# Kernel tuning notes

Hardware: AMD Instinct MI355X
Metric: run time of the kernel (lower is better)

Reference implementation:

```python
import jax, jax.numpy as jnp
import numpy as np

N_NODES = 100000
N_EDGES = 1600000
H_IN = 128
H_OUT = 128
ELU_ALPHA = 0.1


def setup_inputs() -> dict:
    key = jax.random.key(0)
    k = jax.random.split(key, 6)
    x = jax.random.normal(k[0], (N_NODES, H_IN), dtype=jnp.float32)
    edge_index = jax.random.randint(k[1], (2, N_EDGES), 0, N_NODES, dtype=jnp.int64)
    s = 1.0 / np.sqrt(H_IN)
    W_conv = jax.random.uniform(k[2], (H_IN, H_OUT), jnp.float32, -s, s)
    b_conv = jnp.zeros((H_OUT,), jnp.float32)
    W_skip = jax.random.uniform(k[3], (H_IN, H_OUT), jnp.float32, -s, s)
    b_skip = jax.random.uniform(k[4], (H_OUT,), jnp.float32, -s, s)
    return {"x": x, "edge_index": edge_index, "W_conv": W_conv,
            "b_conv": b_conv, "W_skip": W_skip, "b_skip": b_skip}


def reference(x, edge_index, W_conv, b_conv, W_skip, b_skip):
    # GCNConv(improved=True): add self-loops with weight 2.0, symmetric norm.
    N = x.shape[0]
    src, dst = edge_index[0], edge_index[1]
    # degree = incoming edge weights (1.0 each) + 2.0 self-loop weight
    deg = jnp.zeros((N,), x.dtype).at[dst].add(1.0) + 2.0
    dinv = jax.lax.rsqrt(deg)                     # deg >= 2 always
    norm = dinv[src] * dinv[dst]                  # [E]
    h = x @ W_conv                                # [N, H_OUT]
    # scatter-add of normalized messages over real edges
    agg = jax.ops.segment_sum(norm[:, None] * h[src], dst, num_segments=N)
    # self-loop contribution: weight 2 * dinv[i]^2
    agg = agg + (2.0 * dinv * dinv)[:, None] * h
    out = agg + b_conv + x @ W_skip + b_skip
    # Dropout(p=0.1) in eval mode = identity; ELU(alpha=0.1)
    return jnp.where(out > 0, out, ELU_ALPHA * (jnp.exp(out) - 1.0))
```

## Files before the change

### kernel.cpp

```cpp
#include <hip/hip_runtime.h>
#include <hip/hip_bf16.h>
#include <hip/hip_fp16.h>

#define H 128
#define BW 128
#define BSH 7
#define NB 256

typedef __attribute__((ext_vector_type(8))) short short8;
typedef __attribute__((ext_vector_type(4))) float f32x4;

__device__ inline unsigned short f2bf(float f) {
    union { float f; unsigned int u; } v; v.f = f;
    unsigned int r = (v.u + 0x7fffu + ((v.u >> 16) & 1u)) >> 16;
    return (unsigned short)r;
}
__device__ inline float bf2f(unsigned short h) {
    union { unsigned int u; float f; } v; v.u = ((unsigned int)h) << 16;
    return v.f;
}

__global__ __launch_bounds__(256) void quant_hist_kernel(const float* __restrict__ x,
                                                         const float* __restrict__ Wc,
                                                         const float* __restrict__ Ws,
                                                         const int* __restrict__ ei,
                                                         uint* __restrict__ xq,
                                                         float* __restrict__ invs,
                                                         short8* __restrict__ wp,
                                                         int* __restrict__ counts,
                                                         int N, int E, int nbu,
                                                         int chunk, int qb) {
    __shared__ int h[1024];
    if (blockIdx.x >= qb) {
        const int b = blockIdx.x - qb;
        for (int i = threadIdx.x; i < nbu; i += 256) h[i] = 0;
        __syncthreads();
        const int lo = b * chunk;
        const int hi = min(E, lo + chunk);
        for (int e = lo + threadIdx.x; e < hi; e += 256)
            atomicAdd(&h[ei[E + e] >> BSH], 1);
        __syncthreads();
        for (int i = threadIdx.x; i < nbu; i += 256) counts[b * nbu + i] = h[i];
        return;
    }
    int node = blockIdx.x * 8 + (threadIdx.x >> 5);
    if (node < N) {
        int l32 = threadIdx.x & 31;
        float4 v = ((const float4*)x)[node * 32 + l32];
        float m = fmaxf(fmaxf(fabsf(v.x), fabsf(v.y)), fmaxf(fabsf(v.z), fabsf(v.w)));
        #pragma unroll
        for (int mk = 1; mk < 32; mk <<= 1) m = fmaxf(m, __shfl_xor(m, mk));
        m = fmaxf(m, 1e-30f);
        float s = 127.0f / m;
        int q0 = min(255, max(0, (int)rintf(v.x * s) + 128));
        int q1 = min(255, max(0, (int)rintf(v.y * s) + 128));
        int q2 = min(255, max(0, (int)rintf(v.z * s) + 128));
        int q3 = min(255, max(0, (int)rintf(v.w * s) + 128));
        xq[node * 32 + l32] = (uint)q0 | ((uint)q1 << 8) | ((uint)q2 << 16) | ((uint)q3 << 24);
        if (l32 == 0) invs[node] = m / 127.0f;
    }
    if (blockIdx.x < 8) {
        int t = blockIdx.x * 256 + threadIdx.x;
        int lane = t & 63;
        int nt = (t >> 6) & 7;
        int ks = t >> 9;
        int kbase = ks * 32 + (lane >> 4) * 8;
        int col = nt * 16 + (lane & 15);
        short8 whc, whs, wls;
        #pragma unroll
        for (int j = 0; j < 8; ++j) {
            float wc = Wc[(kbase + j) * H + col];
            float ws = Ws[(kbase + j) * H + col];
            unsigned short hc = f2bf(wc);
            unsigned short hs = f2bf(ws);
            whc[j] = (short)hc;
            whs[j] = (short)hs;
            wls[j] = (short)f2bf(ws - bf2f(hs));
        }
        int base = (ks * 8 + nt) * 64 + lane;
        wp[base] = whc;
        wp[2048 + base] = whs;
        wp[4096 + base] = wls;
    }
}

__global__ __launch_bounds__(NB) void p2_scan(const int* __restrict__ counts,
                                              int* __restrict__ scanned,
                                              int* __restrict__ btot, int nbu) {
    __shared__ int s[NB];
    const int k = blockIdx.x, t = threadIdx.x;
    int v = counts[t * nbu + k];
    s[t] = v;
    __syncthreads();
    for (int off = 1; off < NB; off <<= 1) {
        int a = (t >= off) ? s[t - off] : 0;
        __syncthreads();
        s[t] += a;
        __syncthreads();
    }
    scanned[t * nbu + k] = s[t] - v;
    if (t == NB - 1) btot[k] = s[t];
}

__global__ __launch_bounds__(256) void p5_scatter(const int* __restrict__ ei,
                                                  const int* __restrict__ btot,
                                                  const int* __restrict__ scanned,
                                                  int* __restrict__ tmp,
                                                  int* __restrict__ cstart,
                                                  int E, int nbu, int chunk) {
    __shared__ int sc[1024];
    __shared__ int part[256];
    __shared__ int lb[1024];
    const int t = threadIdx.x;
    const int b = blockIdx.x;
    const int base = t * 4;
    int v0 = (base + 0 < nbu) ? btot[base + 0] : 0;
    int v1 = (base + 1 < nbu) ? btot[base + 1] : 0;
    int v2 = (base + 2 < nbu) ? btot[base + 2] : 0;
    int v3 = (base + 3 < nbu) ? btot[base + 3] : 0;
    int s1 = v0 + v1, s2 = s1 + v2, s3 = s2 + v3;
    part[t] = s3;
    __syncthreads();
    for (int off = 1; off < 256; off <<= 1) {
        int a = (t >= off) ? part[t - off] : 0;
        __syncthreads();
        part[t] += a;
        __syncthreads();
    }
    int add = (t > 0) ? part[t - 1] : 0;
    sc[base + 0] = add;
    sc[base + 1] = add + v0;
    sc[base + 2] = add + s1;
    sc[base + 3] = add + s2;
    __syncthreads();
    if (b == 0) {
        for (int k = t; k < nbu; k += 256) cstart[k] = sc[k];
        if (t == 0) cstart[nbu] = E;
    }
    for (int k = t; k < nbu; k += 256) lb[k] = sc[k] + scanned[b * nbu + k];
    __syncthreads();
    const int lo = b * chunk;
    const int hi = min(E, lo + chunk);
    for (int e = lo + t; e < hi; e += 256) {
        int s = ei[e], d = ei[E + e];
        int slot = atomicAdd(&lb[d >> BSH], 1);
        tmp[slot] = ((d & (BW - 1)) << 17) | s;
    }
}

__global__ __launch_bounds__(256) void csra_kernel(const int* __restrict__ tmp,
                                                   const int* __restrict__ cstart,
                                                   const float* __restrict__ invs,
                                                   int* __restrict__ rstart,
                                                   float* __restrict__ dinv,
                                                   float* __restrict__ ainv,
                                                   float* __restrict__ selfw,
                                                   int N, int E) {
    __shared__ int ldeg[BW];
    __shared__ int lscan[BW];
    const int b = blockIdx.x;
    const int nstart = b << BSH;
    const int estart = cstart[b];
    const int eend = cstart[b + 1];
    const int t = threadIdx.x;

    if (t < BW) ldeg[t] = 0;
    __syncthreads();
    for (int i = estart + t; i < eend; i += 256)
        atomicAdd(&ldeg[(tmp[i] >> 17) & (BW - 1)], 1);
    __syncthreads();
    if (t < BW) lscan[t] = ldeg[t];
    __syncthreads();
    #pragma unroll
    for (int off = 1; off < BW; off <<= 1) {
        int a = 0;
        if (t < BW && t >= off) a = lscan[t - off];
        __syncthreads();
        if (t < BW) lscan[t] += a;
        __syncthreads();
    }
    if (t < BW) {
        int excl = lscan[t] - ldeg[t];
        int n = nstart + t;
        if (n < N) {
            float iv = invs[n];
            float dv = rsqrtf((float)ldeg[t] + 2.0f);
            rstart[n] = estart + excl;
            dinv[n] = dv;
            ainv[n] = dv * iv;
            selfw[n] = 2.0f * dv * dv * iv;
        }
    }
    if (b == 0 && t == 0) rstart[N] = E;
}

__global__ __launch_bounds__(256) void csrb_kernel(const int* __restrict__ tmp,
                                                   const int* __restrict__ cstart,
                                                   const int* __restrict__ rstart,
                                                   const float* __restrict__ dinv,
                                                   const float* __restrict__ ainv,
                                                   int* __restrict__ entries,
                                                   unsigned short* __restrict__ wgt,
                                                   int N, int E) {
    __shared__ int lcur[BW];
    __shared__ float ldv[BW];
    const int b = blockIdx.x;
    const int nstart = b << BSH;
    const int t = threadIdx.x;
    if (t < BW) {
        int n = nstart + t;
        lcur[t] = (n < N) ? rstart[n] : 0;
        ldv[t] = (n < N) ? dinv[n] : 0.f;
    }
    __syncthreads();
    const int estart = cstart[b];
    const int eend = cstart[b + 1];
    for (int i = estart + t; i < eend; i += 256) {
        int v = tmp[i];
        int ld = (v >> 17) & (BW - 1);
        int src = v & 0x1FFFF;
        float w = ainv[src] * ldv[ld];
        int slot = atomicAdd(&lcur[ld], 1);
        entries[slot] = src;
        wgt[slot] = __half_as_ushort(__float2half(w));
    }
}

__global__ __launch_bounds__(256) void agg_kernel(const int* __restrict__ entries,
                                                  const unsigned short* __restrict__ wgt,
                                                  const int* __restrict__ rstart,
                                                  const float* __restrict__ selfw,
                                                  const uint* __restrict__ xq,
                                                  unsigned short* __restrict__ z, int N) {
    int node = blockIdx.x * 4 + (threadIdx.x >> 6);
    if (node >= N) return;
    const int lane = threadIdx.x & 63;
    const int l16 = lane & 15;
    const int q4 = lane >> 4;
    const uint2* x2 = (const uint2*)xq;

    int start = rstart[node];
    int end = rstart[node + 1];
    float sw = selfw[node];
    uint2 qs = x2[node * 16 + l16];

    float a0 = 0.f, a1 = 0.f, a2 = 0.f, a3 = 0.f;
    float a4 = 0.f, a5 = 0.f, a6 = 0.f, a7 = 0.f;
    float sumw = 0.f;

    for (int c = start; c < end; c += 64) {
        int rem = end - c;
        int src = 0;
        float w = 0.f;
        if (lane < rem) {
            src = entries[c + lane];
            w = __half2float(__ushort_as_half(wgt[c + lane]));
        }
        int cnt = rem < 64 ? rem : 64;
        int iters = (cnt + 3) >> 2;
        #pragma unroll 4
        for (int t = 0; t < iters; ++t) {
            int idx = 4 * t + q4;
            int ss = __shfl(src, idx);
            float wv = __shfl(w, idx);
            uint2 q = x2[ss * 16 + l16];
            sumw += wv;
            a0 += wv * (float)(q.x & 0xffu);
            a1 += wv * (float)((q.x >> 8) & 0xffu);
            a2 += wv * (float)((q.x >> 16) & 0xffu);
            a3 += wv * (float)(q.x >> 24);
            a4 += wv * (float)(q.y & 0xffu);
            a5 += wv * (float)((q.y >> 8) & 0xffu);
            a6 += wv * (float)((q.y >> 16) & 0xffu);
            a7 += wv * (float)(q.y >> 24);
        }
    }

    #define R2(A) A += __shfl_xor(A, 16); A += __shfl_xor(A, 32);
    R2(a0) R2(a1) R2(a2) R2(a3) R2(a4) R2(a5) R2(a6) R2(a7) R2(sumw)
    #undef R2

    if (q4 == 0) {
        sumw += sw;
        a0 += sw * (float)(qs.x & 0xffu);
        a1 += sw * (float)((qs.x >> 8) & 0xffu);
        a2 += sw * (float)((qs.x >> 16) & 0xffu);
        a3 += sw * (float)(qs.x >> 24);
        a4 += sw * (float)(qs.y & 0xffu);
        a5 += sw * (float)((qs.y >> 8) & 0xffu);
        a6 += sw * (float)((qs.y >> 16) & 0xffu);
        a7 += sw * (float)(qs.y >> 24);
        float off = 128.f * sumw;
        uint4 o;
        o.x = (uint)f2bf(a0 - off) | ((uint)f2bf(a1 - off) << 16);
        o.y = (uint)f2bf(a2 - off) | ((uint)f2bf(a3 - off) << 16);
        o.z = (uint)f2bf(a4 - off) | ((uint)f2bf(a5 - off) << 16);
        o.w = (uint)f2bf(a6 - off) | ((uint)f2bf(a7 - off) << 16);
        ((uint4*)z)[node * 16 + l16] = o;
    }
}

__global__ __launch_bounds__(256) void gemm_kernel(const unsigned short* __restrict__ zb,
                                                   const float* __restrict__ x,
                                                   const short8* __restrict__ wp,
                                                   const float* __restrict__ bc,
                                                   const float* __restrict__ bsk,
                                                   float* __restrict__ out, int N) {
    const int lane = threadIdx.x & 63;
    const int wave = threadIdx.x >> 6;
    const int m = lane & 15;
    const int quad = lane >> 4;
    const int row = blockIdx.x * 64 + wave * 16 + m;
    const bool rowok = row < N;

    f32x4 acc[8];
    #pragma unroll
    for (int i = 0; i < 8; ++i) acc[i] = (f32x4){0.f, 0.f, 0.f, 0.f};

    #pragma unroll
    for (int ks = 0; ks < 4; ++ks) {
        const int k0 = ks * 32 + quad * 8;
        short8 za = {0, 0, 0, 0, 0, 0, 0, 0};
        short8 xa_h = {0, 0, 0, 0, 0, 0, 0, 0};
        short8 xa_l = {0, 0, 0, 0, 0, 0, 0, 0};
        if (rowok) {
            za = ((const short8*)zb)[(row * H + k0) >> 3];
            float4 a = *(const float4*)&x[row * H + k0];
            float4 b = *(const float4*)&x[row * H + k0 + 4];
            float xv[8] = {a.x, a.y, a.z, a.w, b.x, b.y, b.z, b.w};
            #pragma unroll
            for (int j = 0; j < 8; ++j) {
                unsigned short h = f2bf(xv[j]);
                xa_h[j] = (short)h;
                xa_l[j] = (short)f2bf(xv[j] - bf2f(h));
            }
        }
        #pragma unroll
        for (int nt = 0; nt < 8; ++nt) {
            int base = (ks * 8 + nt) * 64 + lane;
            short8 bch = wp[base];
            short8 bsh = wp[2048 + base];
            short8 bsl = wp[4096 + base];
            acc[nt] = __builtin_amdgcn_mfma_f32_16x16x32_bf16(za, bch, acc[nt], 0, 0, 0);
            acc[nt] = __builtin_amdgcn_mfma_f32_16x16x32_bf16(xa_h, bsh, acc[nt], 0, 0, 0);
            acc[nt] = __builtin_amdgcn_mfma_f32_16x16x32_bf16(xa_l, bsh, acc[nt], 0, 0, 0);
            acc[nt] = __builtin_amdgcn_mfma_f32_16x16x32_bf16(xa_h, bsl, acc[nt], 0, 0, 0);
        }
    }

    const int orow_base = blockIdx.x * 64 + wave * 16 + quad * 4;
    #pragma unroll
    for (int nt = 0; nt < 8; ++nt) {
        int col = nt * 16 + m;
        float bias = bc[col] + bsk[col];
        #pragma unroll
        for (int r = 0; r < 4; ++r) {
            int orow = orow_base + r;
            if (orow < N) {
                float v = acc[nt][r] + bias;
                v = v > 0.f ? v : 0.1f * (__expf(v) - 1.f);
                out[orow * H + col] = v;
            }
        }
    }
}

extern "C" void kernel_launch(void* const* d_in, const int* in_sizes, int n_in,
                              void* d_out, int out_size, void* d_ws, size_t ws_size,
                              hipStream_t stream) {
    const float* x   = (const float*)d_in[0];
    const int*   ei  = (const int*)d_in[1];
    const float* Wc  = (const float*)d_in[2];
    const float* bc  = (const float*)d_in[3];
    const float* Wsk = (const float*)d_in[4];
    const float* bsk = (const float*)d_in[5];
    float* out = (float*)d_out;

    const int N = in_sizes[0] / H;
    const int E = in_sizes[1] / 2;
    const int nbu = (N + BW - 1) / BW;
    const int chunk = (E + NB - 1) / NB;
    const int qb = (N + 7) / 8;

    char* w = (char*)d_ws;
    short8*         wp      = (short8*)w;
    int*            rstart  = (int*)(w + 131072);
    float*          selfw   = (float*)(w + 589824);
    int*            entries = (int*)(w + 1048576);
    unsigned short* wgt     = (unsigned short*)(w + 7471104);
    uint*           xq      = (uint*)(w + 10747904);
    unsigned short* z       = (unsigned short*)(w + 23592960);
    float*          invs    = (float*)(w + 23592960);
    float*          dinv    = (float*)(w + 23992960);
    float*          ainv    = (float*)(w + 24392960);
    int*            cstart  = (int*)(w + 24792960);
    int*            btot    = (int*)(w + 24796160);
    int*            counts  = (int*)(w + 24799360);
    int*            scanned = (int*)(w + 25600128);
    int*            tmp     = (int*)(w + 26400896);

    quant_hist_kernel<<<qb + NB, 256, 0, stream>>>(x, Wc, Wsk, ei, xq, invs, wp,
                                                   counts, N, E, nbu, chunk, qb);

    p2_scan<<<nbu, NB, 0, stream>>>(counts, scanned, btot, nbu);
    p5_scatter<<<NB, 256, 0, stream>>>(ei, btot, scanned, tmp, cstart, E, nbu, chunk);
    csra_kernel<<<nbu, 256, 0, stream>>>(tmp, cstart, invs, rstart, dinv, ainv, selfw, N, E);
    csrb_kernel<<<nbu, 256, 0, stream>>>(tmp, cstart, rstart, dinv, ainv, entries, wgt, N, E);

    agg_kernel<<<(N + 3) / 4, 256, 0, stream>>>(entries, wgt, rstart, selfw, xq, z, N);

    gemm_kernel<<<(N + 63) / 64, 256, 0, stream>>>(z, x, wp, bc, bsk, out, N);
}
```

Before: 270.5 us.

## Load neighbor indices directly in aggregation; stage GEMM weights in LDS

The aggregation kernel drops the cooperative per-64-edge load plus shuffle broadcast. Each lane group now reads its edge index and weight straight from global memory, removing the shuffles and the outer chunk loop at the cost of redundant loads across the 16 lanes. The GEMM kernel stages each k-slice of the packed weight fragments into shared memory once per block, so the four waves share one copy instead of each reading it from global/L2. This adds two barriers per k-step.

Result: no change. 274.5 us (+1.5%).

```diff
diff --git a/kernel.cpp b/kernel.cpp
--- a/kernel.cpp
+++ b/kernel.cpp
@@ -248,21 +248,14 @@
     float a4 = 0.f, a5 = 0.f, a6 = 0.f, a7 = 0.f;
     float sumw = 0.f;
 
-    for (int c = start; c < end; c += 64) {
-        int rem = end - c;
-        int src = 0;
-        float w = 0.f;
-        if (lane < rem) {
-            src = entries[c + lane];
-            w = __half2float(__ushort_as_half(wgt[c + lane]));
-        }
-        int cnt = rem < 64 ? rem : 64;
-        int iters = (cnt + 3) >> 2;
-        #pragma unroll 4
-        for (int t = 0; t < iters; ++t) {
-            int idx = 4 * t + q4;
-            int ss = __shfl(src, idx);
-            float wv = __shfl(w, idx);
+    const int deg = end - start;
+    const int iters = (deg + 3) >> 2;
+    #pragma unroll 4
+    for (int t = 0; t < iters; ++t) {
+        int idx = 4 * t + q4;
+        if (idx < deg) {
+            int ss = entries[start + idx];
+            float wv = __half2float(__ushort_as_half(wgt[start + idx]));
             uint2 q = x2[ss * 16 + l16];
             sumw += wv;
             a0 += wv * (float)(q.x & 0xffu);
@@ -306,8 +299,10 @@
                                                    const float* __restrict__ bc,
                                                    const float* __restrict__ bsk,
                                                    float* __restrict__ out, int N) {
-    const int lane = threadIdx.x & 63;
-    const int wave = threadIdx.x >> 6;
+    __shared__ short8 bsm[1536];
+    const int tid = threadIdx.x;
+    const int lane = tid & 63;
+    const int wave = tid >> 6;
     const int m = lane & 15;
     const int quad = lane >> 4;
     const int row = blockIdx.x * 64 + wave * 16 + m;
@@ -335,12 +330,18 @@
                 xa_l[j] = (short)f2bf(xv[j] - bf2f(h));
             }
         }
+        __syncthreads();
+        #pragma unroll
+        for (int p = 0; p < 3; ++p) {
+            bsm[p * 512 + tid]       = wp[p * 2048 + ks * 512 + tid];
+            bsm[p * 512 + 256 + tid] = wp[p * 2048 + ks * 512 + 256 + tid];
+        }
+        __syncthreads();
         #pragma unroll
         for (int nt = 0; nt < 8; ++nt) {
-            int base = (ks * 8 + nt) * 64 + lane;
-            short8 bch = wp[base];
-            short8 bsh = wp[2048 + base];
-            short8 bsl = wp[4096 + base];
+            short8 bch = bsm[nt * 64 + lane];
+            short8 bsh = bsm[512 + nt * 64 + lane];
+            short8 bsl = bsm[1024 + nt * 64 + lane];
             acc[nt] = __builtin_amdgcn_mfma_f32_16x16x32_bf16(za, bch, acc[nt], 0, 0, 0);
             acc[nt] = __builtin_amdgcn_mfma_f32_16x16x32_bf16(xa_h, bsh, acc[nt], 0, 0, 0);
             acc[nt] = __builtin_amdgcn_mfma_f32_16x16x32_bf16(xa_l, bsh, acc[nt], 0, 0, 0);
```
